# Optimization experiments

Measured on AMD Instinct MI355X. Metric: run time of the kernel, lower is better.

## Reference

```python
import jax, jax.numpy as jnp
import numpy as np

B, T, I, H, O = 128, 512, 256, 512, 256


def setup_inputs() -> dict:
    key = jax.random.key(0)
    ks = jax.random.split(key, 12)
    s = 1.0 / np.sqrt(H)  # torch nn.GRUCell/Linear-style uniform init scale
    u = lambda k, shape: jax.random.uniform(k, shape, jnp.float32, -s, s)
    return {
        "x": jax.random.normal(ks[0], (B, T, I), jnp.float32),
        "h0": jax.random.normal(ks[1], (B, H), jnp.float32),
        "W_ih0": u(ks[2], (3 * H, I)),
        "W_hh0": u(ks[3], (3 * H, H)),
        "b_ih0": u(ks[4], (3 * H,)),
        "b_hh0": u(ks[5], (3 * H,)),
        "W_ih1": u(ks[6], (3 * H, H)),
        "W_hh1": u(ks[7], (3 * H, H)),
        "b_ih1": u(ks[8], (3 * H,)),
        "b_hh1": u(ks[9], (3 * H,)),
        "W_out": u(ks[10], (O, H)),
        "b_out": u(ks[11], (O,)),
    }


def _cell(inp, h, W_ih, W_hh, b_ih, b_hh):
    # Standard GRU cell (PyTorch gate order: r, z, n)
    gi = inp @ W_ih.T + b_ih  # [B, 3H]
    gh = h @ W_hh.T + b_hh    # [B, 3H]
    i_r, i_z, i_n = jnp.split(gi, 3, axis=-1)
    h_r, h_z, h_n = jnp.split(gh, 3, axis=-1)
    r = jax.nn.sigmoid(i_r + h_r)
    z = jax.nn.sigmoid(i_z + h_z)
    n = jnp.tanh(i_n + r * h_n)
    return (1.0 - z) * n + z * h


def reference(x, h0, W_ih0, W_hh0, b_ih0, b_hh0, W_ih1, W_hh1, b_ih1, b_hh1, W_out, b_out):
    def step(h, x_t):
        h = _cell(x_t, h, W_ih0, W_hh0, b_ih0, b_hh0)
        # Source quirk: a SINGLE hidden state is shared across stacked layers,
        # so layer 1 receives h both as input and as previous hidden state.
        h = _cell(h, h, W_ih1, W_hh1, b_ih1, b_hh1)
        y = h @ W_out.T + b_out  # [B, O]
        return h, y

    _, Y = jax.lax.scan(step, h0, jnp.swapaxes(x, 0, 1))  # Y: [T, B, O]
    return jnp.swapaxes(Y, 0, 1)  # [B, T, O]
```

## Files before the change

kernel.cpp:

```cpp
#include <hip/hip_runtime.h>


typedef short s16x8 __attribute__((ext_vector_type(8)));
typedef float f32x4 __attribute__((ext_vector_type(4)));
typedef unsigned short u16;
typedef unsigned int u32;

#define MFMA(a, b, c) __builtin_amdgcn_mfma_f32_16x16x32_bf16((a), (b), (c), 0, 0, 0)

static constexpr int NBLK = 128;
static constexpr int LDS_WROWS = 112;
static constexpr int LDS_STRIDE = 520;
static constexpr int LDS_BYTES = LDS_WROWS * LDS_STRIDE * 2 + 2 * 512 * 4;
static constexpr int FLAGS_U32 = 8192;

__device__ __forceinline__ u16 f2bf(float f) {
  unsigned u = __builtin_bit_cast(unsigned, f);
  u = u + 0x7fffu + ((u >> 16) & 1u);
  return (u16)(u >> 16);
}
__device__ __forceinline__ float sigm(float x) { return 1.f / (1.f + __expf(-x)); }
__device__ __forceinline__ float tanh_f(float x) { return 1.f - 2.f / (1.f + __expf(2.f * x)); }

__device__ __forceinline__ s16x8 scload16(const u16* p) {
  s16x8 v;
  asm volatile("global_load_dwordx4 %0, %1, off sc0 sc1" : "=v"(v) : "v"(p));
  return v;
}
__device__ __forceinline__ void scstore_u16(u16* p, u16 v) {
  unsigned vv = v;
  asm volatile("global_store_short %0, %1, off sc0 sc1" :: "v"(p), "v"(vv) : "memory");
}
#define VWAIT0()                                        \
  do {                                                  \
    asm volatile("s_waitcnt vmcnt(0)" ::: "memory");    \
    __builtin_amdgcn_sched_barrier(0);                  \
  } while (0)

__device__ __forceinline__ void fbar(u32* fbase, int s, u32 val) {
  asm volatile("s_waitcnt vmcnt(0)" ::: "memory");
  __syncthreads();
  if (threadIdx.x == 0) {
    asm volatile("global_store_dword %0, %1, off sc0 sc1"
                 :: "v"(fbase + s * 32), "v"(val) : "memory");
  }
  if (threadIdx.x < 64) {
    const int lane = threadIdx.x;
    const u32* p = fbase + lane * 32;
    for (;;) {
      int ok = 1;
      if (lane < 32) {
        u32 v;
        asm volatile("global_load_dword %0, %1, off sc0 sc1\n\ts_waitcnt vmcnt(0)"
                     : "=v"(v) : "v"(p) : "memory");
        ok = (v >= val) ? 1 : 0;
      }
      if (__all(ok)) break;
      __builtin_amdgcn_s_sleep(4);
    }
  }
  __syncthreads();
}

__global__ void prep_kernel(const float* __restrict__ W_ih0, const float* __restrict__ W_hh0,
                            const float* __restrict__ W_ih1, const float* __restrict__ W_hh1,
                            const float* __restrict__ W_out, const float* __restrict__ h0,
                            u16* __restrict__ WL0, u16* __restrict__ WL1,
                            u16* __restrict__ WOB, u16* __restrict__ ring1,
                            u32* __restrict__ flags) {
  const int n0 = 1536 * 768, n1 = 2048 * 512, n2 = 256 * 512, n3 = 128 * 512;
  const int total = n0 + n1 + n2 + n3 + FLAGS_U32;
  for (int i = blockIdx.x * blockDim.x + threadIdx.x; i < total; i += gridDim.x * blockDim.x) {
    if (i < n0) {
      int row = i / 768, c = i % 768;
      float v = (c < 256) ? W_ih0[row * 256 + c] : W_hh0[row * 512 + (c - 256)];
      WL0[i] = f2bf(v);
    } else if (i < n0 + n1) {
      int k2 = i - n0;
      int row = k2 / 512, k = k2 % 512;
      int strip = row >> 9, j = row & 511;
      float v;
      if (strip == 0)      v = W_ih1[j * 512 + k] + W_hh1[j * 512 + k];
      else if (strip == 1) v = W_ih1[(512 + j) * 512 + k] + W_hh1[(512 + j) * 512 + k];
      else if (strip == 2) v = W_ih1[(1024 + j) * 512 + k];
      else                 v = W_hh1[(1024 + j) * 512 + k];
      WL1[k2] = f2bf(v);
    } else if (i < n0 + n1 + n2) {
      int k2 = i - n0 - n1;
      WOB[k2] = f2bf(W_out[k2]);
    } else if (i < n0 + n1 + n2 + n3) {
      int k2 = i - n0 - n1 - n2;
      ring1[k2] = f2bf(h0[k2]);
    } else {
      flags[i - n0 - n1 - n2 - n3] = 0u;
    }
  }
}

__global__ __launch_bounds__(256) void gru_persist(
    const float* __restrict__ x, const float* __restrict__ h0,
    const float* __restrict__ b_ih0, const float* __restrict__ b_hh0,
    const float* __restrict__ b_ih1, const float* __restrict__ b_hh1,
    const float* __restrict__ b_out,
    const u16* __restrict__ WL0, const u16* __restrict__ WL1, const u16* __restrict__ WOB,
    u16* __restrict__ ring,
    u16* __restrict__ hlb,
    float* __restrict__ Y, u32* __restrict__ flagsA, u32* __restrict__ flagsB) {
  extern __shared__ u16 smem[];
  float* h_f32  = (float*)(smem + LDS_WROWS * LDS_STRIDE);
  float* hl_f32 = h_f32 + 512;

  const int blk = blockIdx.x;
  const int m = blk >> 5;
  const int s = blk & 31;
  const int w = threadIdx.x >> 6, l = threadIdx.x & 63;
  const int l15 = l & 15, l4 = l >> 4;

  for (int idx = threadIdx.x; idx < LDS_WROWS * 512; idx += 256) {
    int row = idx >> 9, k = idx & 511;
    u16 v;
    if (row < 48) {
      int g = row >> 4, jj = row & 15;
      v = WL0[(size_t)(g * 512 + s * 16 + jj) * 768 + 256 + k];
    } else {
      int rr = row - 48, g = rr >> 4, jj = rr & 15;
      v = WL1[(size_t)(g * 512 + s * 16 + jj) * 512 + k];
    }
    smem[row * LDS_STRIDE + k] = v;
  }
  for (int idx = threadIdx.x; idx < 512; idx += 256) {
    int rr = idx >> 4, cc = idx & 15;
    h_f32[idx] = h0[(size_t)(32 * m + rr) * 512 + s * 16 + cc];
  }
  __syncthreads();

  const int jg = s * 16 + l15;
  const float br0 = b_ih0[jg] + b_hh0[jg];
  const float bz0 = b_ih0[512 + jg] + b_hh0[512 + jg];
  const float bni0 = b_ih0[1024 + jg], bnh0 = b_hh0[1024 + jg];
  const float br1 = b_ih1[jg] + b_hh1[jg];
  const float bz1 = b_ih1[512 + jg] + b_hh1[512 + jg];
  const float bni1 = b_ih1[1024 + jg], bnh1 = b_hh1[1024 + jg];

  const u16* wxr = WL0 + (size_t)jg * 768 + l4 * 8;
  const u16* wxz = WL0 + (size_t)(512 + jg) * 768 + l4 * 8;
  const u16* wxn = WL0 + (size_t)(1024 + jg) * 768 + l4 * 8;
  const u16* lr  = smem + (0 * 16 + l15) * LDS_STRIDE + l4 * 8;
  const u16* lz  = smem + (1 * 16 + l15) * LDS_STRIDE + l4 * 8;
  const u16* ln  = smem + (2 * 16 + l15) * LDS_STRIDE + l4 * 8;
  const u16* m10 = smem + (48 + 0 * 16 + l15) * LDS_STRIDE + l4 * 8;
  const u16* m11 = smem + (48 + 1 * 16 + l15) * LDS_STRIDE + l4 * 8;
  const u16* m12 = smem + (48 + 2 * 16 + l15) * LDS_STRIDE + l4 * 8;
  const u16* m13 = smem + (48 + 3 * 16 + l15) * LDS_STRIDE + l4 * 8;

  const int amt = w & 1;
  const int bmt = (w - 2) & 1;
  const int arow = 32 * m + amt * 16 + l15;
  const int brow = 32 * m + bmt * 16 + l15;

  const int yo = (s & 15) * 16 + l15;
  const float ybo = b_out[yo];
  const u16* ywv = WOB + (size_t)yo * 512 + l4 * 8;

  u32* fA = flagsA + m * 1024;
  u32* fB = flagsB + m * 1024;

  for (int t = 0; t < 512; ++t) {
    const u16* ringc = ring + (size_t)((t + 1) & 1) * 65536;
    u16* ringn = ring + (size_t)(t & 1) * 65536;

    if (w < 2) {
      s16x8 hb[16];
      const u16* hr = ringc + (size_t)arow * 512 + l4 * 8;
      #pragma unroll
      for (int kt = 0; kt < 16; ++kt) hb[kt] = scload16(hr + kt * 32);

      f32x4 aR = {0,0,0,0}, aZ = {0,0,0,0}, aNI = {0,0,0,0}, aNH = {0,0,0,0};
      const float* xr = x + ((size_t)arow * 512 + t) * 256 + l4 * 8;
      #pragma unroll
      for (int kt = 0; kt < 8; ++kt) {
        float4 u = *(const float4*)(xr + kt * 32);
        float4 v = *(const float4*)(xr + kt * 32 + 4);
        s16x8 a;
        a[0]=f2bf(u.x); a[1]=f2bf(u.y); a[2]=f2bf(u.z); a[3]=f2bf(u.w);
        a[4]=f2bf(v.x); a[5]=f2bf(v.y); a[6]=f2bf(v.z); a[7]=f2bf(v.w);
        aR  = MFMA(a, *(const s16x8*)(wxr + kt * 32), aR);
        aZ  = MFMA(a, *(const s16x8*)(wxz + kt * 32), aZ);
        aNI = MFMA(a, *(const s16x8*)(wxn + kt * 32), aNI);
      }
      VWAIT0();
      #pragma unroll
      for (int kt = 0; kt < 16; ++kt) {
        aR  = MFMA(hb[kt], *(const s16x8*)(lr + kt * 32), aR);
        aZ  = MFMA(hb[kt], *(const s16x8*)(lz + kt * 32), aZ);
        aNH = MFMA(hb[kt], *(const s16x8*)(ln + kt * 32), aNH);
      }

      if (s < 16 && t > 0) {
        f32x4 acc = {0,0,0,0};
        #pragma unroll
        for (int kt = 0; kt < 16; ++kt)
          acc = MFMA(hb[kt], *(const s16x8*)(ywv + kt * 32), acc);
        #pragma unroll
        for (int j = 0; j < 4; ++j)
          Y[((size_t)(32 * m + amt * 16 + l4 * 4 + j) * 512 + (t - 1)) * 256 + yo]
              = acc[j] + ybo;
      }

      #pragma unroll
      for (int j = 0; j < 4; ++j) {
        int rr = amt * 16 + l4 * 4 + j;
        float r = sigm(aR[j] + br0), z = sigm(aZ[j] + bz0);
        float n = tanh_f(aNI[j] + bni0 + r * (aNH[j] + bnh0));
        float h = (1.f - z) * n + z * h_f32[rr * 16 + l15];
        hl_f32[rr * 16 + l15] = h;
        scstore_u16(hlb + (size_t)(32 * m + rr) * 512 + jg, f2bf(h));
      }
    }
    fbar(fA, s, (u32)(t + 1));

    if (w >= 2) {
      s16x8 pb[16];
      const u16* ar = hlb + (size_t)brow * 512 + l4 * 8;
      #pragma unroll
      for (int kt = 0; kt < 16; ++kt) pb[kt] = scload16(ar + kt * 32);
      VWAIT0();
      f32x4 cR = {0,0,0,0}, cZ = {0,0,0,0}, cNI = {0,0,0,0}, cNH = {0,0,0,0};
      #pragma unroll
      for (int kt = 0; kt < 16; ++kt) {
        cR  = MFMA(pb[kt], *(const s16x8*)(m10 + kt * 32), cR);
        cZ  = MFMA(pb[kt], *(const s16x8*)(m11 + kt * 32), cZ);
        cNI = MFMA(pb[kt], *(const s16x8*)(m12 + kt * 32), cNI);
        cNH = MFMA(pb[kt], *(const s16x8*)(m13 + kt * 32), cNH);
      }
      #pragma unroll
      for (int j = 0; j < 4; ++j) {
        int rr = bmt * 16 + l4 * 4 + j;
        float r = sigm(cR[j] + br1), z = sigm(cZ[j] + bz1);
        float n = tanh_f(cNI[j] + bni1 + r * (cNH[j] + bnh1));
        float h = (1.f - z) * n + z * hl_f32[rr * 16 + l15];
        h_f32[rr * 16 + l15] = h;
        scstore_u16(ringn + (size_t)(32 * m + rr) * 512 + jg, f2bf(h));
      }
    }
    fbar(fB, s, (u32)(t + 1));
  }

  if (w < 2 && s < 16) {
    const u16* Hf = ring + 65536;
    s16x8 yb[16];
    const u16* ar = Hf + (size_t)arow * 512 + l4 * 8;
    #pragma unroll
    for (int kt = 0; kt < 16; ++kt) yb[kt] = scload16(ar + kt * 32);
    VWAIT0();
    f32x4 acc = {0,0,0,0};
    #pragma unroll
    for (int kt = 0; kt < 16; ++kt)
      acc = MFMA(yb[kt], *(const s16x8*)(ywv + kt * 32), acc);
    #pragma unroll
    for (int j = 0; j < 4; ++j)
      Y[((size_t)(32 * m + amt * 16 + l4 * 4 + j) * 512 + 511) * 256 + yo]
          = acc[j] + ybo;
  }
}

extern "C" void kernel_launch(void* const* d_in, const int* in_sizes, int n_in,
                              void* d_out, int out_size, void* d_ws, size_t ws_size,
                              hipStream_t stream) {
  const float* x     = (const float*)d_in[0];
  const float* h0    = (const float*)d_in[1];
  const float* W_ih0 = (const float*)d_in[2];
  const float* W_hh0 = (const float*)d_in[3];
  const float* b_ih0 = (const float*)d_in[4];
  const float* b_hh0 = (const float*)d_in[5];
  const float* W_ih1 = (const float*)d_in[6];
  const float* W_hh1 = (const float*)d_in[7];
  const float* b_ih1 = (const float*)d_in[8];
  const float* b_hh1 = (const float*)d_in[9];
  const float* W_out = (const float*)d_in[10];
  const float* b_out = (const float*)d_in[11];
  float* Y = (float*)d_out;

  u32* flagsA = (u32*)d_ws;
  u32* flagsB = flagsA + 4096;
  u16* WL0  = (u16*)(flagsA + FLAGS_U32);
  u16* WL1  = WL0 + 1536 * 768;
  u16* WOB  = WL1 + 2048 * 512;
  u16* ring = WOB + 256 * 512;
  u16* hlb  = ring + 2 * 65536;

  (void)hipFuncSetAttribute((const void*)gru_persist,
                            hipFuncAttributeMaxDynamicSharedMemorySize, LDS_BYTES);

  prep_kernel<<<dim3(1024), dim3(256), 0, stream>>>(W_ih0, W_hh0, W_ih1, W_hh1,
                                                    W_out, h0, WL0, WL1, WOB,
                                                    ring + 65536, flagsA);
  gru_persist<<<dim3(NBLK), dim3(256), LDS_BYTES, stream>>>(
      x, h0, b_ih0, b_hh0, b_ih1, b_hh1, b_out, WL0, WL1, WOB,
      ring, hlb, Y, flagsA, flagsB);
}
```

Measured before the change: 7.042 ms.

## Replace block-wide flag barriers with per-wave flags and leader-gathered go signals

Drops the two block-wide global barriers per timestep, each of which made every block poll all 32 peers. Layer-0 and layer-1 waves now post their own per-wave flags and run in separate loops. Block s==0 of each group gathers all 64 flags and broadcasts a go signal that the other blocks poll. The output projection also moves after the layer-0 flag store, so it overlaps with layer 1's wait. The risks are extra latency through the leader hop and subtle cross-wave ordering bugs, since hl_f32 and h_f32 in LDS are now shared between waves without __syncthreads.

```diff
diff --git a/kernel.cpp b/kernel.cpp
--- a/kernel.cpp
+++ b/kernel.cpp
@@ -12,7 +12,8 @@
 static constexpr int LDS_WROWS = 112;
 static constexpr int LDS_STRIDE = 520;
 static constexpr int LDS_BYTES = LDS_WROWS * LDS_STRIDE * 2 + 2 * 512 * 4;
-static constexpr int FLAGS_U32 = 8192;
+static constexpr int OFF_FA = 0, OFF_FB = 8192, OFF_GA = 16384, OFF_GB = 17408;
+static constexpr int FLAGS_U32 = 18432;
 
 __device__ __forceinline__ u16 f2bf(float f) {
   unsigned u = __builtin_bit_cast(unsigned, f);
@@ -30,36 +31,40 @@
 __device__ __forceinline__ void scstore_u16(u16* p, u16 v) {
   unsigned vv = v;
   asm volatile("global_store_short %0, %1, off sc0 sc1" :: "v"(p), "v"(vv) : "memory");
+}
+__device__ __forceinline__ u32 scload_u32(const u32* p) {
+  u32 v;
+  asm volatile("global_load_dword %0, %1, off sc0 sc1\n\ts_waitcnt vmcnt(0)"
+               : "=v"(v) : "v"(p) : "memory");
+  return v;
+}
+__device__ __forceinline__ void scstore_u32(u32* p, u32 v) {
+  asm volatile("global_store_dword %0, %1, off sc0 sc1" :: "v"(p), "v"(v) : "memory");
 }
 #define VWAIT0()                                        \
   do {                                                  \
     asm volatile("s_waitcnt vmcnt(0)" ::: "memory");    \
     __builtin_amdgcn_sched_barrier(0);                  \
   } while (0)
-
-__device__ __forceinline__ void fbar(u32* fbase, int s, u32 val) {
-  asm volatile("s_waitcnt vmcnt(0)" ::: "memory");
-  __syncthreads();
-  if (threadIdx.x == 0) {
-    asm volatile("global_store_dword %0, %1, off sc0 sc1"
-                 :: "v"(fbase + s * 32), "v"(val) : "memory");
-  }
-  if (threadIdx.x < 64) {
-    const int lane = threadIdx.x;
-    const u32* p = fbase + lane * 32;
-    for (;;) {
-      int ok = 1;
-      if (lane < 32) {
-        u32 v;
-        asm volatile("global_load_dword %0, %1, off sc0 sc1\n\ts_waitcnt vmcnt(0)"
-                     : "=v"(v) : "v"(p) : "memory");
-        ok = (v >= val) ? 1 : 0;
-      }
-      if (__all(ok)) break;
-      __builtin_amdgcn_s_sleep(4);
-    }
-  }
-  __syncthreads();
+#define DRAIN_ALL()                                              \
+  do {                                                           \
+    asm volatile("s_waitcnt vmcnt(0) lgkmcnt(0)" ::: "memory");  \
+    __builtin_amdgcn_sched_barrier(0);                           \
+  } while (0)
+
+__device__ __forceinline__ void gather64(const u32* base, u32 val, int l) {
+  for (;;) {
+    u32 v = scload_u32(base + l * 32);
+    if (__all(v >= val)) break;
+    __builtin_amdgcn_s_sleep(2);
+  }
+}
+__device__ __forceinline__ void pollgo(const u32* p, u32 val) {
+  for (;;) {
+    u32 v = scload_u32(p);
+    if (v >= val) break;
+    __builtin_amdgcn_s_sleep(4);
+  }
 }
 
 __global__ void prep_kernel(const float* __restrict__ W_ih0, const float* __restrict__ W_hh0,
@@ -105,7 +110,7 @@
     const u16* __restrict__ WL0, const u16* __restrict__ WL1, const u16* __restrict__ WOB,
     u16* __restrict__ ring,
     u16* __restrict__ hlb,
-    float* __restrict__ Y, u32* __restrict__ flagsA, u32* __restrict__ flagsB) {
+    float* __restrict__ Y, u32* __restrict__ flags) {
   extern __shared__ u16 smem[];
   float* h_f32  = (float*)(smem + LDS_WROWS * LDS_STRIDE);
   float* hl_f32 = h_f32 + 512;
@@ -153,23 +158,33 @@
   const u16* m12 = smem + (48 + 2 * 16 + l15) * LDS_STRIDE + l4 * 8;
   const u16* m13 = smem + (48 + 3 * 16 + l15) * LDS_STRIDE + l4 * 8;
 
-  const int amt = w & 1;
-  const int bmt = (w - 2) & 1;
-  const int arow = 32 * m + amt * 16 + l15;
-  const int brow = 32 * m + bmt * 16 + l15;
-
-  const int yo = (s & 15) * 16 + l15;
-  const float ybo = b_out[yo];
-  const u16* ywv = WOB + (size_t)yo * 512 + l4 * 8;
-
-  u32* fA = flagsA + m * 1024;
-  u32* fB = flagsB + m * 1024;
-
-  for (int t = 0; t < 512; ++t) {
-    const u16* ringc = ring + (size_t)((t + 1) & 1) * 65536;
-    u16* ringn = ring + (size_t)(t & 1) * 65536;
-
-    if (w < 2) {
+  u32* fA = flags + OFF_FA + m * 2048;
+  u32* fB = flags + OFF_FB + m * 2048;
+  u32* gA = flags + OFF_GA + m * 256;
+  u32* gB = flags + OFF_GB + m * 256;
+
+  if (w < 2) {
+    const int amt = w;
+    const int arow = 32 * m + amt * 16 + l15;
+    u32* myfA = fA + (s * 2 + amt) * 32;
+    const u32* mygo = gB + (s & 7) * 32;
+    const int yo = (s & 15) * 16 + l15;
+    const float ybo = b_out[yo];
+    const u16* ywv = WOB + (size_t)yo * 512 + l4 * 8;
+
+    for (int t = 0; t < 512; ++t) {
+      const u16* ringc = ring + (size_t)((t + 1) & 1) * 65536;
+
+      if (t > 0) {
+        if (s == 0) {
+          gather64(fB, (u32)t, l);
+          if (w == 0 && l < 8) scstore_u32(gB + l * 32, (u32)t);
+        } else {
+          pollgo(mygo, (u32)t);
+        }
+        __builtin_amdgcn_sched_barrier(0);
+      }
+
       s16x8 hb[16];
       const u16* hr = ringc + (size_t)arow * 512 + l4 * 8;
       #pragma unroll
@@ -196,6 +211,18 @@
         aNH = MFMA(hb[kt], *(const s16x8*)(ln + kt * 32), aNH);
       }
 
+      #pragma unroll
+      for (int j = 0; j < 4; ++j) {
+        int rr = amt * 16 + l4 * 4 + j;
+        float r = sigm(aR[j] + br0), z = sigm(aZ[j] + bz0);
+        float n = tanh_f(aNI[j] + bni0 + r * (aNH[j] + bnh0));
+        float h = (1.f - z) * n + z * h_f32[rr * 16 + l15];
+        hl_f32[rr * 16 + l15] = h;
+        scstore_u16(hlb + (size_t)(32 * m + rr) * 512 + jg, f2bf(h));
+      }
+      DRAIN_ALL();
+      if (l == 0) scstore_u32(myfA, (u32)(t + 1));
+
       if (s < 16 && t > 0) {
         f32x4 acc = {0,0,0,0};
         #pragma unroll
@@ -206,20 +233,47 @@
           Y[((size_t)(32 * m + amt * 16 + l4 * 4 + j) * 512 + (t - 1)) * 256 + yo]
               = acc[j] + ybo;
       }
-
-      #pragma unroll
-      for (int j = 0; j < 4; ++j) {
-        int rr = amt * 16 + l4 * 4 + j;
-        float r = sigm(aR[j] + br0), z = sigm(aZ[j] + bz0);
-        float n = tanh_f(aNI[j] + bni0 + r * (aNH[j] + bnh0));
-        float h = (1.f - z) * n + z * h_f32[rr * 16 + l15];
-        hl_f32[rr * 16 + l15] = h;
-        scstore_u16(hlb + (size_t)(32 * m + rr) * 512 + jg, f2bf(h));
-      }
-    }
-    fbar(fA, s, (u32)(t + 1));
-
-    if (w >= 2) {
+    }
+
+    if (s == 0) {
+      gather64(fB, 512u, l);
+      if (w == 0 && l < 8) scstore_u32(gB + l * 32, 512u);
+    } else {
+      pollgo(mygo, 512u);
+    }
+    if (s < 16) {
+      const u16* Hf = ring + 65536;
+      s16x8 yb[16];
+      const u16* ar = Hf + (size_t)arow * 512 + l4 * 8;
+      #pragma unroll
+      for (int kt = 0; kt < 16; ++kt) yb[kt] = scload16(ar + kt * 32);
+      VWAIT0();
+      f32x4 acc = {0,0,0,0};
+      #pragma unroll
+      for (int kt = 0; kt < 16; ++kt)
+        acc = MFMA(yb[kt], *(const s16x8*)(ywv + kt * 32), acc);
+      #pragma unroll
+      for (int j = 0; j < 4; ++j)
+        Y[((size_t)(32 * m + amt * 16 + l4 * 4 + j) * 512 + 511) * 256 + yo]
+            = acc[j] + ybo;
+    }
+  } else {
+    const int bmt = w - 2;
+    const int brow = 32 * m + bmt * 16 + l15;
+    u32* myfB = fB + (s * 2 + bmt) * 32;
+    const u32* mygo = gA + (s & 7) * 32;
+
+    for (int t = 0; t < 512; ++t) {
+      u16* ringn = ring + (size_t)(t & 1) * 65536;
+
+      if (s == 0) {
+        gather64(fA, (u32)(t + 1), l);
+        if (w == 2 && l < 8) scstore_u32(gA + l * 32, (u32)(t + 1));
+      } else {
+        pollgo(mygo, (u32)(t + 1));
+      }
+      __builtin_amdgcn_sched_barrier(0);
+
       s16x8 pb[16];
       const u16* ar = hlb + (size_t)brow * 512 + l4 * 8;
       #pragma unroll
@@ -242,25 +296,9 @@
         h_f32[rr * 16 + l15] = h;
         scstore_u16(ringn + (size_t)(32 * m + rr) * 512 + jg, f2bf(h));
       }
-    }
-    fbar(fB, s, (u32)(t + 1));
-  }
-
-  if (w < 2 && s < 16) {
-    const u16* Hf = ring + 65536;
-    s16x8 yb[16];
-    const u16* ar = Hf + (size_t)arow * 512 + l4 * 8;
-    #pragma unroll
-    for (int kt = 0; kt < 16; ++kt) yb[kt] = scload16(ar + kt * 32);
-    VWAIT0();
-    f32x4 acc = {0,0,0,0};
-    #pragma unroll
-    for (int kt = 0; kt < 16; ++kt)
-      acc = MFMA(yb[kt], *(const s16x8*)(ywv + kt * 32), acc);
-    #pragma unroll
-    for (int j = 0; j < 4; ++j)
-      Y[((size_t)(32 * m + amt * 16 + l4 * 4 + j) * 512 + 511) * 256 + yo]
-          = acc[j] + ybo;
+      DRAIN_ALL();
+      if (l == 0) scstore_u32(myfB, (u32)(t + 1));
+    }
   }
 }
 
@@ -281,9 +319,8 @@
   const float* b_out = (const float*)d_in[11];
   float* Y = (float*)d_out;
 
-  u32* flagsA = (u32*)d_ws;
-  u32* flagsB = flagsA + 4096;
-  u16* WL0  = (u16*)(flagsA + FLAGS_U32);
+  u32* flags = (u32*)d_ws;
+  u16* WL0  = (u16*)(flags + FLAGS_U32);
   u16* WL1  = WL0 + 1536 * 768;
   u16* WOB  = WL1 + 2048 * 512;
   u16* ring = WOB + 256 * 512;
@@ -294,8 +331,8 @@
 
   prep_kernel<<<dim3(1024), dim3(256), 0, stream>>>(W_ih0, W_hh0, W_ih1, W_hh1,
                                                     W_out, h0, WL0, WL1, WOB,
-                                                    ring + 65536, flagsA);
+                                                    ring + 65536, flags);
   gru_persist<<<dim3(NBLK), dim3(256), LDS_BYTES, stream>>>(
       x, h0, b_ih0, b_hh0, b_ih1, b_hh1, b_out, WL0, WL1, WOB,
-      ring, hlb, Y, flagsA, flagsB);
-}
+      ring, hlb, Y, flags);
+}
```

Measured after the change: 5.639 ms (median of 2 runs). -19.9%, faster.
